# Kernel tuning notes

Measured on AMD Instinct MI355X. Metric: run time of the kernel, lower is better.

## Reference

```python
import jax, jax.numpy as jnp
import numpy as np

N, T, F, H, NH, OUT = 4096, 32, 7, 64, 8, 8


def setup_inputs() -> dict:
    key = jax.random.key(0)
    ks = jax.random.split(key, 24)
    def nrm(k, shape, scale):
        return jax.random.normal(k, shape, jnp.float32) * scale
    s_gru = 1.0 / np.sqrt(H)
    s_gat = 1.0 / np.sqrt(NH * OUT)
    s_lin = 0.05
    return {
        "inputs": jax.random.normal(ks[0], (N, T, F), jnp.float32),
        "adj": jax.random.randint(ks[1], (N, N), 0, 2, jnp.int32),
        "W_ih": nrm(ks[2], (3 * H, F), s_gru),
        "W_hh": nrm(ks[3], (3 * H, H), s_gru),
        "b_ih": nrm(ks[4], (3 * H,), s_gru),
        "b_hh": nrm(ks[5], (3 * H,), s_gru),
        "gat_w": nrm(ks[6], (H, NH * OUT), s_gat),
        "gat_wu": nrm(ks[7], (NH, OUT, 1), 1.0),
        "gat_wv": nrm(ks[8], (NH, OUT, 1), 1.0),
        "gat_bias": nrm(ks[9], (1, NH * OUT), s_gat),
        "proj_w": nrm(ks[10], (NH * OUT, H), s_lin),
        "proj_b": nrm(ks[11], (NH * OUT,), s_lin),
        "mlp_self_w": nrm(ks[12], (H, H), s_lin),
        "mlp_self_b": nrm(ks[13], (H,), s_lin),
        "mlp_pos_w": nrm(ks[14], (H, NH * OUT), s_lin),
        "mlp_pos_b": nrm(ks[15], (H,), s_lin),
        "sem_w1": nrm(ks[16], (H, H), s_lin),
        "sem_b1": nrm(ks[17], (H,), s_lin),
        "sem_w2": nrm(ks[18], (1, H), s_lin),
        "pred_w": nrm(ks[19], (1, H), s_lin),
        "pred_b": nrm(ks[20], (1,), s_lin),
    }


def reference(inputs, adj, W_ih, W_hh, b_ih, b_hh, gat_w, gat_wu, gat_wv,
              gat_bias, proj_w, proj_b, mlp_self_w, mlp_self_b,
              mlp_pos_w, mlp_pos_b, sem_w1, sem_b1, sem_w2, pred_w, pred_b):
    n = inputs.shape[0]
    # --- GRU encoder (batch_first, 1 layer); take final hidden state ---
    gx = jnp.einsum('ntf,gf->tng', inputs, W_ih) + b_ih  # [T, N, 3H]
    h0 = jnp.zeros((n, W_hh.shape[1]), inputs.dtype)

    def step(h, g):
        gh = h @ W_hh.T + b_hh
        gxr, gxz, gxn = jnp.split(g, 3, axis=-1)
        ghr, ghz, ghn = jnp.split(gh, 3, axis=-1)
        r = jax.nn.sigmoid(gxr + ghr)
        z = jax.nn.sigmoid(gxz + ghz)
        nn_ = jnp.tanh(gxn + r * ghn)
        return (1.0 - z) * nn_ + z * h, None

    h, _ = jax.lax.scan(step, h0, gx)  # [N, H]

    # --- multi-head GAT over dense adjacency ---
    sup = (h @ gat_w).reshape(n, NH, OUT).transpose(1, 0, 2)  # [nh, N, out]
    f1 = jnp.einsum('hnd,hdo->hn', sup, gat_wu)[:, None, :]   # [nh, 1, N]
    f2 = jnp.einsum('hnd,hdo->hn', sup, gat_wv)[:, :, None]   # [nh, N, 1]
    logits = jax.nn.leaky_relu(f1 + f2, negative_slope=0.2)   # [nh, N, N]
    adjf = adj.astype(logits.dtype)[None]                     # [1, N, N]
    mw = logits * adjf
    ex = jnp.exp(mw - jnp.max(mw, axis=2, keepdims=True)) * (adjf > 0)
    attn = ex / jnp.clip(jnp.sum(ex, axis=2, keepdims=True), 1e-10)
    pos = jnp.einsum('hij,hjd->hid', attn, sup)               # [nh, N, out]
    pos = pos.transpose(1, 0, 2).reshape(n, NH * OUT)
    pos = pos + gat_bias + h @ proj_w.T + proj_b              # bias + residual proj

    # --- stack self/pos channels, PairNorm (mode='PN') ---
    s = jnp.stack([h @ mlp_self_w.T + mlp_self_b,
                   pos @ mlp_pos_w.T + mlp_pos_b], axis=1)    # [N, 2, H]
    s = s - s.mean(axis=0)
    rownorm_mean = jnp.sqrt(1e-6 + jnp.mean(jnp.sum(s * s, axis=1)))
    s = s / rownorm_mean

    # --- semantic attention over the 2 channels ---
    w = jnp.tanh(s @ sem_w1.T + sem_b1) @ sem_w2.T            # [N, 2, 1]
    we = jnp.exp(w - jnp.max(w, axis=1, keepdims=True))
    beta = we / (jnp.sum(we, axis=1, keepdims=True) + 1e-10)
    emb = jnp.sum(beta * s, axis=1)                           # [N, H]

    # --- predictor ---
    return jax.nn.sigmoid(emb @ pred_w.T + pred_b)            # [N, 1]
```

## Files before the change

### kernel.cpp

```cpp
#include <hip/hip_runtime.h>
#include <math.h>

#define NN 4096
#define TT 32
#define FF 7
#define HH 64
#define NHEAD 8
#define DOUT 8
#define LOG2E 1.44269504f

#if __has_builtin(__builtin_amdgcn_exp2f)
#define EXP2(x) __builtin_amdgcn_exp2f(x)
#else
#define EXP2(x) exp2f(x)
#endif

typedef short bf16x8 __attribute__((ext_vector_type(8)));
typedef float f32x4 __attribute__((ext_vector_type(4)));

__device__ __forceinline__ float sigm(float x){
  x = fminf(fmaxf(x, -30.f), 30.f);
  return 1.f / (1.f + __expf(-x));
}
__device__ __forceinline__ float tanh_fast(float x){
  x = fminf(fmaxf(x, -15.f), 15.f);
  float e = __expf(2.f*x);
  return (e - 1.f) / (e + 1.f);
}
__device__ __forceinline__ unsigned short bf16rne(float f){
  unsigned u = __float_as_uint(f);
  u += 0x7fffu + ((u >> 16) & 1u);
  return (unsigned short)(u >> 16);
}
__device__ __forceinline__ unsigned bfpack2(float a, float b){
  return (unsigned)bf16rne(a) | ((unsigned)bf16rne(b) << 16);
}
__device__ __forceinline__ unsigned cvtpk_bf16(float a, float b){
  unsigned r;
  asm("v_cvt_pk_bf16_f32 %0, %1, %2" : "=v"(r) : "v"(a), "v"(b));
  return r;
}

__global__ __launch_bounds__(256) void k0_prep(
    const float* __restrict__ pw, const float* __restrict__ msw,
    const float* __restrict__ mpw, const float* __restrict__ sw1,
    const float* __restrict__ Wih, const float* __restrict__ Whh,
    const float* __restrict__ bih, const float* __restrict__ bhh,
    float* __restrict__ wtproj, float* __restrict__ wtself,
    float* __restrict__ wtpos, float* __restrict__ wtsem,
    uint4* __restrict__ whhF, uint4* __restrict__ wihF)
{
  if (blockIdx.x < 16){
    int tid = threadIdx.x + blockIdx.x*256;
    int d = tid >> 6, k = tid & 63;
    wtproj[k*64+d] = pw[tid];
    wtself[k*64+d] = msw[tid];
    wtpos[k*64+d]  = mpw[tid];
    wtsem[k*64+d]  = sw1[tid];
    return;
  }
  int idx = (blockIdx.x-16)*256 + threadIdx.x;
  if (idx < 24*64){
    int f = idx >> 6, lane = idx & 63;
    int T = f >> 1, c = f & 1;
    int g = T*16 + (lane & 15);
    const float* wp = Whh + g*64 + c*32 + (lane >> 4)*8;
    uint4 v;
    v.x = bfpack2(wp[0], wp[1]);
    v.y = bfpack2(wp[2], wp[3]);
    v.z = bfpack2(wp[4], wp[5]);
    v.w = bfpack2(wp[6], wp[7]);
    whhF[idx] = v;
  } else if (idx < 36*64){
    int i2 = idx - 24*64;
    int T = i2 >> 6, lane = i2 & 63;
    int g = T*16 + (lane & 15);
    int kg = lane >> 4;
    float bias = (T < 8) ? (bih[g] + bhh[g]) : bih[g];
    float f8[8];
    #pragma unroll
    for (int j = 0; j < 8; ++j){
      int k = kg*8 + j;
      f8[j] = (k < 7) ? Wih[g*7 + k] : ((k == 7) ? bias : 0.f);
    }
    uint4 v;
    v.x = bfpack2(f8[0], f8[1]); v.y = bfpack2(f8[2], f8[3]);
    v.z = bfpack2(f8[4], f8[5]); v.w = bfpack2(f8[6], f8[7]);
    wihF[i2] = v;
  }
}

__global__ __launch_bounds__(256) void k1_fused(
    const float* __restrict__ x,
    const uint4* __restrict__ whhF,
    const uint4* __restrict__ wihF,
    const float* __restrict__ bhh,
    float* __restrict__ hout,
    const int* __restrict__ adj,
    unsigned long long* __restrict__ adjmT)
{
  __shared__ __align__(16) short s_xb[32][16][8];
  __shared__ __align__(16) short s_hb[2][16][72];

  int tid = threadIdx.x;
  int lane = tid & 63, w = tid >> 6;

  if (blockIdx.x >= 256){
    int row = (blockIdx.x - 256)*4 + w;
    const int* ap = adj + (size_t)row*NN;
    size_t base = (size_t)(row >> 4)*1024 + (row & 15);
    #pragma unroll 8
    for (int s = 0; s < 64; ++s){
      unsigned long long m = __ballot(ap[s*64 + lane] != 0);
      if (lane == 0) adjmT[base + s*16] = m;
    }
    return;
  }

  int nb = blockIdx.x * 16;
  int row = lane & 15;
  int kg  = lane >> 4;

  union U { bf16x8 v; uint4 q; };
  U u;
  u.q = wihF[w*64 + lane];           bf16x8 fRx  = u.v;
  u.q = whhF[(w*2+0)*64 + lane];     bf16x8 fRh0 = u.v;
  u.q = whhF[(w*2+1)*64 + lane];     bf16x8 fRh1 = u.v;
  u.q = wihF[(4+w)*64 + lane];       bf16x8 fZx  = u.v;
  u.q = whhF[((4+w)*2+0)*64 + lane]; bf16x8 fZh0 = u.v;
  u.q = whhF[((4+w)*2+1)*64 + lane]; bf16x8 fZh1 = u.v;
  u.q = wihF[(8+w)*64 + lane];       bf16x8 fNx  = u.v;
  u.q = whhF[((8+w)*2+0)*64 + lane]; bf16x8 fNh0 = u.v;
  u.q = whhF[((8+w)*2+1)*64 + lane]; bf16x8 fNh1 = u.v;

  for (int s = tid; s < 4096; s += 256){
    int t = s >> 7, node = (s >> 3) & 15, k = s & 7;
    float v = (k < 7) ? x[(size_t)(nb + node)*224 + t*7 + k] : ((k == 7) ? 1.f : 0.f);
    s_xb[t][node][k] = (short)bf16rne(v);
  }
  for (int i = tid; i < 576; i += 256) ((unsigned*)&s_hb[0][0][0])[i] = 0u;

  float bhn_[4];
  #pragma unroll
  for (int j = 0; j < 4; ++j) bhn_[j] = bhh[128 + w*16 + kg*4 + j];
  float hreg[4] = {0.f, 0.f, 0.f, 0.f};
  f32x4 z4 = {0.f, 0.f, 0.f, 0.f};

  __syncthreads();
  int cur = 0;
  for (int t = 0; t < TT; ++t){
    bf16x8 bx = {0,0,0,0,0,0,0,0};
    if (lane < 16) bx = *(const bf16x8*)&s_xb[t][row][0];
    bf16x8 bh0 = *(const bf16x8*)&s_hb[cur][row][kg*8];
    bf16x8 bh1 = *(const bf16x8*)&s_hb[cur][row][32 + kg*8];

    f32x4 aR = __builtin_amdgcn_mfma_f32_16x16x32_bf16(fRx, bx, z4, 0, 0, 0);
    aR = __builtin_amdgcn_mfma_f32_16x16x32_bf16(fRh0, bh0, aR, 0, 0, 0);
    aR = __builtin_amdgcn_mfma_f32_16x16x32_bf16(fRh1, bh1, aR, 0, 0, 0);
    f32x4 aZ = __builtin_amdgcn_mfma_f32_16x16x32_bf16(fZx, bx, z4, 0, 0, 0);
    aZ = __builtin_amdgcn_mfma_f32_16x16x32_bf16(fZh0, bh0, aZ, 0, 0, 0);
    aZ = __builtin_amdgcn_mfma_f32_16x16x32_bf16(fZh1, bh1, aZ, 0, 0, 0);
    f32x4 aNx = __builtin_amdgcn_mfma_f32_16x16x32_bf16(fNx, bx, z4, 0, 0, 0);
    f32x4 aNh = __builtin_amdgcn_mfma_f32_16x16x32_bf16(fNh0, bh0, z4, 0, 0, 0);
    aNh = __builtin_amdgcn_mfma_f32_16x16x32_bf16(fNh1, bh1, aNh, 0, 0, 0);

    #pragma unroll
    for (int j = 0; j < 4; ++j){
      float rr = sigm(aR[j]);
      float zz = sigm(aZ[j]);
      float nn = tanh_fast(aNx[j] + rr*(aNh[j] + bhn_[j]));
      hreg[j] = (1.f - zz)*nn + zz*hreg[j];
    }
    uint2 p;
    p.x = bfpack2(hreg[0], hreg[1]);
    p.y = bfpack2(hreg[2], hreg[3]);
    *(uint2*)&s_hb[cur^1][row][w*16 + kg*4] = p;
    __syncthreads();
    cur ^= 1;
  }

  #pragma unroll
  for (int j = 0; j < 4; ++j)
    hout[(size_t)(nb + row)*64 + w*16 + kg*4 + j] = hreg[j];
}

__global__ __launch_bounds__(256) void k2_sup(
    const float* __restrict__ h, const float* __restrict__ gat_w,
    const float* __restrict__ wu, const float* __restrict__ wv,
    unsigned short* __restrict__ supbJ,
    float* __restrict__ f1t,
    float* __restrict__ f2)
{
  int tid = threadIdx.x;
  int wave = tid >> 6, lane = tid & 63;
  int n = blockIdx.x*4 + wave;
  float hreg = h[n*64 + lane];
  float acc = 0.f;
  #pragma unroll
  for (int k = 0; k < 64; ++k){
    float hk = __shfl(hreg, k, 64);
    acc += hk * gat_w[k*64 + lane];
  }
  int hh = lane >> 3, o = lane & 7;
  supbJ[(size_t)hh*32768 + (n>>3)*64 + o*8 + (n&7)] = bf16rne(acc);
  float p1 = acc * wu[lane];
  float p2 = acc * wv[lane];
  #pragma unroll
  for (int s = 1; s < 8; s <<= 1){
    p1 += __shfl_xor(p1, s, 64);
    p2 += __shfl_xor(p2, s, 64);
  }
  if (o == 0){
    f1t[(size_t)hh*NN + n] = p1 * LOG2E;
    f2[n*8 + hh] = p2 * LOG2E;
  }
}

__global__ __launch_bounds__(256) void k3_gat(
    const unsigned long long* __restrict__ adjmT,
    const unsigned short* __restrict__ supbJ,
    const float* __restrict__ f1t,
    const float* __restrict__ f2,
    float* __restrict__ posg)
{
  __shared__ f32x4 s_acc[4][64];
  int tid = threadIdx.x;
  int lane = tid & 63, js = tid >> 6;
  int gid = blockIdx.x;
  int ib = gid >> 3, h = gid & 7;
  int i0 = ib*16;
  int col = lane & 15;
  int kg  = lane >> 4;

  float f2v = f2[(size_t)(i0+col)*8 + h];

  const unsigned long long* mrowT = adjmT + (size_t)ib*1024;
  const float* f1p = f1t + (size_t)h*NN;
  const unsigned short* bsrcJ = supbJ + (size_t)h*32768;
  unsigned bge8 = (col >= 8) ? 0xffffffffu : 0u;

  f32x4 acc = {0.f, 0.f, 0.f, 0.f};

  #pragma unroll 4
  for (int cc = 0; cc < 32; ++cc){
    int c = js*32 + cc;
    int j8 = c*32 + kg*8;
    unsigned long long mw = mrowT[(c >> 1)*16 + col];
    unsigned mb = (unsigned)(mw >> (((c & 1) << 5) + (kg << 3)));
    float4 fa = *(const float4*)(f1p + j8);
    float4 fb = *(const float4*)(f1p + j8 + 4);

    float p[8];
    p[0]=fa.x; p[1]=fa.y; p[2]=fa.z; p[3]=fa.w;
    p[4]=fb.x; p[5]=fb.y; p[6]=fb.z; p[7]=fb.w;
    #pragma unroll
    for (int e = 0; e < 8; ++e){
      float ls = p[e] + f2v;
      float lrs = fmaxf(ls, 0.2f*ls);
      float pe = EXP2(lrs);
      p[e] = (mb & (1u << e)) ? pe : 0.f;
    }
    union { bf16x8 v; unsigned u[4]; } A;
    A.u[0] = cvtpk_bf16(p[0], p[1]);
    A.u[1] = cvtpk_bf16(p[2], p[3]);
    A.u[2] = cvtpk_bf16(p[4], p[5]);
    A.u[3] = cvtpk_bf16(p[6], p[7]);

    union { bf16x8 v; uint4 q; } B;
    uint4 ld = *(const uint4*)(bsrcJ + (size_t)(c*4 + kg)*64 + (col & 7)*8);
    B.q.x = bge8 ? 0x3f803f80u : ld.x;
    B.q.y = bge8 ? 0x3f803f80u : ld.y;
    B.q.z = bge8 ? 0x3f803f80u : ld.z;
    B.q.w = bge8 ? 0x3f803f80u : ld.w;

    acc = __builtin_amdgcn_mfma_f32_16x16x32_bf16(A.v, B.v, acc, 0, 0, 0);
  }

  s_acc[js][lane] = acc;
  __syncthreads();
  if (js == 0){
    f32x4 a1 = s_acc[1][lane], a2 = s_acc[2][lane], a3 = s_acc[3][lane];
    #pragma unroll
    for (int j = 0; j < 4; ++j) acc[j] += a1[j] + a2[j] + a3[j];

    int slane = (lane & 48) + 8;
    #pragma unroll
    for (int r4 = 0; r4 < 4; ++r4){
      float sv = __shfl(acc[r4], slane, 64);
      float inv = 1.f / fmaxf(sv, 1e-10f);
      if (col < 8)
        posg[(size_t)(i0 + kg*4 + r4)*64 + h*8 + col] = acc[r4] * inv;
    }
  }
}

__global__ __launch_bounds__(256) void k4_mix(
    const float* __restrict__ h, const float* __restrict__ posg,
    const float* __restrict__ gat_bias, const float* __restrict__ proj_b,
    const float* __restrict__ wtproj, const float* __restrict__ wtself,
    const float* __restrict__ wtpos,
    const float* __restrict__ mlp_self_b, const float* __restrict__ mlp_pos_b,
    float* __restrict__ s0, float* __restrict__ s1, float* __restrict__ part)
{
  int tid = threadIdx.x;
  int wave = tid >> 6, lane = tid & 63;
  int n = blockIdx.x*4 + wave;
  float hreg = h[n*64 + lane];
  float pr = proj_b[lane];
  float se = mlp_self_b[lane];
  #pragma unroll
  for (int k = 0; k < 64; ++k){
    float hk = __shfl(hreg, k, 64);
    pr += hk * wtproj[k*64 + lane];
    se += hk * wtself[k*64 + lane];
  }
  float posf = posg[n*64 + lane] + gat_bias[lane] + pr;
  float s1v = mlp_pos_b[lane];
  #pragma unroll
  for (int k = 0; k < 64; ++k){
    float pk = __shfl(posf, k, 64);
    s1v += pk * wtpos[k*64 + lane];
  }
  s0[n*64+lane] = se;
  s1[n*64+lane] = s1v;

  __shared__ float sb0[4][64];
  __shared__ float sb1[4][64];
  __shared__ float sq[4];
  sb0[wave][lane] = se;
  sb1[wave][lane] = s1v;
  float q = se*se + s1v*s1v;
  #pragma unroll
  for (int s = 1; s < 64; s <<= 1) q += __shfl_xor(q, s, 64);
  if (lane == 0) sq[wave] = q;
  __syncthreads();
  if (tid < 64){
    part[blockIdx.x*130 + tid] = sb0[0][tid]+sb0[1][tid]+sb0[2][tid]+sb0[3][tid];
  } else if (tid < 128){
    int d = tid - 64;
    part[blockIdx.x*130 + 64 + d] = sb1[0][d]+sb1[1][d]+sb1[2][d]+sb1[3][d];
  } else if (tid == 128){
    part[blockIdx.x*130 + 128] = sq[0]+sq[1]+sq[2]+sq[3];
  }
}

__global__ __launch_bounds__(1024) void k5_stats(const float* __restrict__ part, float* __restrict__ stats)
{
  int tid = threadIdx.x;
  __shared__ float s_mu[8][128];
  __shared__ float s_sq[8];
  int c = tid & 127, ch = tid >> 7;
  float a = 0.f;
  for (int b = ch*128; b < ch*128+128; ++b) a += part[b*130 + c];
  s_mu[ch][c] = a;
  if (tid < 8){
    float q = 0.f;
    for (int b = tid*128; b < tid*128+128; ++b) q += part[b*130 + 128];
    s_sq[tid] = q;
  }
  __syncthreads();
  if (tid < 128){
    float m = 0.f;
    #pragma unroll
    for (int j = 0; j < 8; ++j) m += s_mu[j][tid];
    s_mu[0][tid] = m;
    stats[tid] = m / 4096.f;
  }
  __syncthreads();
  if (tid == 0){
    float sq = 0.f;
    #pragma unroll
    for (int j = 0; j < 8; ++j) sq += s_sq[j];
    float mu2 = 0.f;
    for (int i = 0; i < 128; ++i){ float m = s_mu[0][i] / 4096.f; mu2 += m*m; }
    float msq = sq/(4096.f*64.f) - mu2/64.f;
    stats[128] = 1.f / sqrtf(1e-6f + msq);
  }
}

__global__ __launch_bounds__(256) void k6_sem(
    const float* __restrict__ s0, const float* __restrict__ s1,
    const float* __restrict__ stats, const float* __restrict__ wtsem,
    const float* __restrict__ sem_b1, const float* __restrict__ sem_w2,
    const float* __restrict__ pred_w, const float* __restrict__ pred_b,
    float* __restrict__ out)
{
  int tid = threadIdx.x;
  int wave = tid >> 6, lane = tid & 63;
  int n = blockIdx.x*4 + wave;
  float rinv = stats[128];
  float a0 = (s0[n*64+lane] - stats[lane]) * rinv;
  float a1 = (s1[n*64+lane] - stats[64+lane]) * rinv;
  float t0 = sem_b1[lane], t1 = t0;
  #pragma unroll
  for (int k = 0; k < 64; ++k){
    float w = wtsem[k*64 + lane];
    t0 += __shfl(a0, k, 64) * w;
    t1 += __shfl(a1, k, 64) * w;
  }
  t0 = tanh_fast(t0); t1 = tanh_fast(t1);
  float w2 = sem_w2[lane];
  float w0 = t0*w2, w1 = t1*w2;
  #pragma unroll
  for (int s = 1; s < 64; s <<= 1){
    w0 += __shfl_xor(w0, s, 64);
    w1 += __shfl_xor(w1, s, 64);
  }
  float mx = fmaxf(w0, w1);
  float e0 = __expf(w0 - mx), e1 = __expf(w1 - mx);
  float denom = e0 + e1 + 1e-10f;
  float b0 = e0/denom, b1 = e1/denom;
  float emb = b0*a0 + b1*a1;
  float pl = emb * pred_w[lane];
  #pragma unroll
  for (int s = 1; s < 64; s <<= 1) pl += __shfl_xor(pl, s, 64);
  if (lane == 0) out[n] = sigm(pl + pred_b[0]);
}

extern "C" void kernel_launch(void* const* d_in, const int* in_sizes, int n_in,
                              void* d_out, int out_size, void* d_ws, size_t ws_size,
                              hipStream_t stream)
{
  (void)in_sizes; (void)n_in; (void)out_size; (void)ws_size;
  const float* x         = (const float*)d_in[0];
  const int*   adj       = (const int*)d_in[1];
  const float* W_ih      = (const float*)d_in[2];
  const float* W_hh      = (const float*)d_in[3];
  const float* b_ih      = (const float*)d_in[4];
  const float* b_hh      = (const float*)d_in[5];
  const float* gat_w     = (const float*)d_in[6];
  const float* gat_wu    = (const float*)d_in[7];
  const float* gat_wv    = (const float*)d_in[8];
  const float* gat_bias  = (const float*)d_in[9];
  const float* proj_w    = (const float*)d_in[10];
  const float* proj_b    = (const float*)d_in[11];
  const float* mlp_self_w= (const float*)d_in[12];
  const float* mlp_self_b= (const float*)d_in[13];
  const float* mlp_pos_w = (const float*)d_in[14];
  const float* mlp_pos_b = (const float*)d_in[15];
  const float* sem_w1    = (const float*)d_in[16];
  const float* sem_b1    = (const float*)d_in[17];
  const float* sem_w2    = (const float*)d_in[18];
  const float* pred_w    = (const float*)d_in[19];
  const float* pred_b    = (const float*)d_in[20];
  float* out = (float*)d_out;
  float* ws  = (float*)d_ws;

  float* h     = ws + 0;
  unsigned short* supbJ = (unsigned short*)(ws + 262144);
  float* f1t   = ws + 393216;
  float* f2    = ws + 425984;
  uint4* whhF  = (uint4*)(ws + 458752);
  uint4* wihF  = (uint4*)(ws + 464896);
  float* posg  = ws + 589824;
  float* s0    = ws + 851968;
  float* s1    = ws + 1114112;
  unsigned long long* adjmT = (unsigned long long*)(ws + 851968);
  float* part  = ws + 1376256;
  float* stats = ws + 1517576;
  float* wtproj= ws + 1517712;
  float* wtself= wtproj + 4096;
  float* wtpos = wtself + 4096;
  float* wtsem = wtpos  + 4096;

  k0_prep<<<25, 256, 0, stream>>>(proj_w, mlp_self_w, mlp_pos_w, sem_w1,
                                  W_ih, W_hh, b_ih, b_hh,
                                  wtproj, wtself, wtpos, wtsem, whhF, wihF);
  k1_fused<<<1280, 256, 0, stream>>>(x, whhF, wihF, b_hh, h, adj, adjmT);
  k2_sup<<<1024, 256, 0, stream>>>(h, gat_w, gat_wu, gat_wv, supbJ, f1t, f2);
  k3_gat<<<2048, 256, 0, stream>>>(adjmT, supbJ, f1t, f2, posg);
  k4_mix<<<1024, 256, 0, stream>>>(h, posg, gat_bias, proj_b, wtproj, wtself, wtpos,
                                   mlp_self_b, mlp_pos_b, s0, s1, part);
  k5_stats<<<1, 1024, 0, stream>>>(part, stats);
  k6_sem<<<1024, 256, 0, stream>>>(s0, s1, stats, wtsem, sem_b1, sem_w2, pred_w, pred_b, out);
}
```

Measured before the change: 148.1 us.

## Run GRU recurrence in one wave per block and simplify GAT B-operand load

The GRU part of k1_fused now has a single wave hold all the recurrent and input weight fragments in registers and compute all four gate tiles itself. This removes the per-timestep __syncthreads and the double-buffered hidden state, at the cost of each wave doing four times the MFMA and activation work, with three of the four waves exiting early. In k3_gat, the per-element select that swapped in constant ones for the upper 8 columns is replaced by a pointer select into a small ones buffer written by k0_prep, so every lane does a plain vector load. The risks are lower parallelism in the latency-bound GRU loop and heavy register pressure from 36 resident fragments.

```diff
diff --git a/kernel.cpp b/kernel.cpp
--- a/kernel.cpp
+++ b/kernel.cpp
@@ -48,7 +48,8 @@
     const float* __restrict__ bih, const float* __restrict__ bhh,
     float* __restrict__ wtproj, float* __restrict__ wtself,
     float* __restrict__ wtpos, float* __restrict__ wtsem,
-    uint4* __restrict__ whhF, uint4* __restrict__ wihF)
+    uint4* __restrict__ whhF, uint4* __restrict__ wihF,
+    unsigned* __restrict__ onesb)
 {
   if (blockIdx.x < 16){
     int tid = threadIdx.x + blockIdx.x*256;
@@ -59,6 +60,7 @@
     wtsem[k*64+d]  = sw1[tid];
     return;
   }
+  if (blockIdx.x == 16 && threadIdx.x < 32) onesb[threadIdx.x] = 0x3f803f80u;
   int idx = (blockIdx.x-16)*256 + threadIdx.x;
   if (idx < 24*64){
     int f = idx >> 6, lane = idx & 63;
@@ -90,7 +92,7 @@
   }
 }
 
-__global__ __launch_bounds__(256) void k1_fused(
+__global__ __launch_bounds__(256, 1) void k1_fused(
     const float* __restrict__ x,
     const uint4* __restrict__ whhF,
     const uint4* __restrict__ wihF,
@@ -100,7 +102,7 @@
     unsigned long long* __restrict__ adjmT)
 {
   __shared__ __align__(16) short s_xb[32][16][8];
-  __shared__ __align__(16) short s_hb[2][16][72];
+  __shared__ __align__(16) short s_hb[16][72];
 
   int tid = threadIdx.x;
   int lane = tid & 63, w = tid >> 6;
@@ -118,70 +120,85 @@
   }
 
   int nb = blockIdx.x * 16;
-  int row = lane & 15;
-  int kg  = lane >> 4;
-
-  union U { bf16x8 v; uint4 q; };
-  U u;
-  u.q = wihF[w*64 + lane];           bf16x8 fRx  = u.v;
-  u.q = whhF[(w*2+0)*64 + lane];     bf16x8 fRh0 = u.v;
-  u.q = whhF[(w*2+1)*64 + lane];     bf16x8 fRh1 = u.v;
-  u.q = wihF[(4+w)*64 + lane];       bf16x8 fZx  = u.v;
-  u.q = whhF[((4+w)*2+0)*64 + lane]; bf16x8 fZh0 = u.v;
-  u.q = whhF[((4+w)*2+1)*64 + lane]; bf16x8 fZh1 = u.v;
-  u.q = wihF[(8+w)*64 + lane];       bf16x8 fNx  = u.v;
-  u.q = whhF[((8+w)*2+0)*64 + lane]; bf16x8 fNh0 = u.v;
-  u.q = whhF[((8+w)*2+1)*64 + lane]; bf16x8 fNh1 = u.v;
 
   for (int s = tid; s < 4096; s += 256){
     int t = s >> 7, node = (s >> 3) & 15, k = s & 7;
     float v = (k < 7) ? x[(size_t)(nb + node)*224 + t*7 + k] : ((k == 7) ? 1.f : 0.f);
     s_xb[t][node][k] = (short)bf16rne(v);
   }
-  for (int i = tid; i < 576; i += 256) ((unsigned*)&s_hb[0][0][0])[i] = 0u;
-
-  float bhn_[4];
-  #pragma unroll
-  for (int j = 0; j < 4; ++j) bhn_[j] = bhh[128 + w*16 + kg*4 + j];
-  float hreg[4] = {0.f, 0.f, 0.f, 0.f};
+  for (int i = tid; i < 576; i += 256) ((unsigned*)&s_hb[0][0])[i] = 0u;
+  __syncthreads();
+  if (w != 0) return;
+
+  int row = lane & 15;
+  int kg  = lane >> 4;
+
+  union U { bf16x8 v; uint4 q; };
+  bf16x8 whh_f[24];
+  #pragma unroll
+  for (int i = 0; i < 24; ++i){ U u; u.q = whhF[i*64 + lane]; whh_f[i] = u.v; }
+  bf16x8 wih_f[12];
+  #pragma unroll
+  for (int i = 0; i < 12; ++i){ U u; u.q = wihF[i*64 + lane]; wih_f[i] = u.v; }
+  #pragma unroll
+  for (int i = 0; i < 24; ++i) asm volatile("" : "+v"(whh_f[i]));
+  #pragma unroll
+  for (int i = 0; i < 12; ++i) asm volatile("" : "+v"(wih_f[i]));
+
+  float bhn_[4][4];
+  #pragma unroll
+  for (int T = 0; T < 4; ++T)
+    #pragma unroll
+    for (int j = 0; j < 4; ++j)
+      bhn_[T][j] = bhh[128 + T*16 + kg*4 + j];
+
+  float hreg[4][4];
+  #pragma unroll
+  for (int T = 0; T < 4; ++T)
+    #pragma unroll
+    for (int j = 0; j < 4; ++j) hreg[T][j] = 0.f;
+
   f32x4 z4 = {0.f, 0.f, 0.f, 0.f};
 
-  __syncthreads();
-  int cur = 0;
   for (int t = 0; t < TT; ++t){
     bf16x8 bx = {0,0,0,0,0,0,0,0};
     if (lane < 16) bx = *(const bf16x8*)&s_xb[t][row][0];
-    bf16x8 bh0 = *(const bf16x8*)&s_hb[cur][row][kg*8];
-    bf16x8 bh1 = *(const bf16x8*)&s_hb[cur][row][32 + kg*8];
-
-    f32x4 aR = __builtin_amdgcn_mfma_f32_16x16x32_bf16(fRx, bx, z4, 0, 0, 0);
-    aR = __builtin_amdgcn_mfma_f32_16x16x32_bf16(fRh0, bh0, aR, 0, 0, 0);
-    aR = __builtin_amdgcn_mfma_f32_16x16x32_bf16(fRh1, bh1, aR, 0, 0, 0);
-    f32x4 aZ = __builtin_amdgcn_mfma_f32_16x16x32_bf16(fZx, bx, z4, 0, 0, 0);
-    aZ = __builtin_amdgcn_mfma_f32_16x16x32_bf16(fZh0, bh0, aZ, 0, 0, 0);
-    aZ = __builtin_amdgcn_mfma_f32_16x16x32_bf16(fZh1, bh1, aZ, 0, 0, 0);
-    f32x4 aNx = __builtin_amdgcn_mfma_f32_16x16x32_bf16(fNx, bx, z4, 0, 0, 0);
-    f32x4 aNh = __builtin_amdgcn_mfma_f32_16x16x32_bf16(fNh0, bh0, z4, 0, 0, 0);
-    aNh = __builtin_amdgcn_mfma_f32_16x16x32_bf16(fNh1, bh1, aNh, 0, 0, 0);
-
-    #pragma unroll
-    for (int j = 0; j < 4; ++j){
-      float rr = sigm(aR[j]);
-      float zz = sigm(aZ[j]);
-      float nn = tanh_fast(aNx[j] + rr*(aNh[j] + bhn_[j]));
-      hreg[j] = (1.f - zz)*nn + zz*hreg[j];
-    }
-    uint2 p;
-    p.x = bfpack2(hreg[0], hreg[1]);
-    p.y = bfpack2(hreg[2], hreg[3]);
-    *(uint2*)&s_hb[cur^1][row][w*16 + kg*4] = p;
-    __syncthreads();
-    cur ^= 1;
-  }
-
-  #pragma unroll
-  for (int j = 0; j < 4; ++j)
-    hout[(size_t)(nb + row)*64 + w*16 + kg*4 + j] = hreg[j];
+    bf16x8 bh0 = *(const bf16x8*)&s_hb[row][kg*8];
+    bf16x8 bh1 = *(const bf16x8*)&s_hb[row][32 + kg*8];
+
+    #pragma unroll
+    for (int Tr = 0; Tr < 4; ++Tr){
+      f32x4 aR = __builtin_amdgcn_mfma_f32_16x16x32_bf16(wih_f[Tr], bx, z4, 0, 0, 0);
+      aR = __builtin_amdgcn_mfma_f32_16x16x32_bf16(whh_f[Tr*2+0], bh0, aR, 0, 0, 0);
+      aR = __builtin_amdgcn_mfma_f32_16x16x32_bf16(whh_f[Tr*2+1], bh1, aR, 0, 0, 0);
+      f32x4 aZ = __builtin_amdgcn_mfma_f32_16x16x32_bf16(wih_f[4+Tr], bx, z4, 0, 0, 0);
+      aZ = __builtin_amdgcn_mfma_f32_16x16x32_bf16(whh_f[(4+Tr)*2+0], bh0, aZ, 0, 0, 0);
+      aZ = __builtin_amdgcn_mfma_f32_16x16x32_bf16(whh_f[(4+Tr)*2+1], bh1, aZ, 0, 0, 0);
+      f32x4 aNx = __builtin_amdgcn_mfma_f32_16x16x32_bf16(wih_f[8+Tr], bx, z4, 0, 0, 0);
+      f32x4 aNh = __builtin_amdgcn_mfma_f32_16x16x32_bf16(whh_f[(8+Tr)*2+0], bh0, z4, 0, 0, 0);
+      aNh = __builtin_amdgcn_mfma_f32_16x16x32_bf16(whh_f[(8+Tr)*2+1], bh1, aNh, 0, 0, 0);
+      #pragma unroll
+      for (int j = 0; j < 4; ++j){
+        float rr = sigm(aR[j]);
+        float zz = sigm(aZ[j]);
+        float nn = tanh_fast(aNx[j] + rr*(aNh[j] + bhn_[Tr][j]));
+        hreg[Tr][j] = (1.f - zz)*nn + zz*hreg[Tr][j];
+      }
+    }
+    #pragma unroll
+    for (int Tr = 0; Tr < 4; ++Tr){
+      uint2 p;
+      p.x = bfpack2(hreg[Tr][0], hreg[Tr][1]);
+      p.y = bfpack2(hreg[Tr][2], hreg[Tr][3]);
+      *(uint2*)&s_hb[row][Tr*16 + kg*4] = p;
+    }
+  }
+
+  #pragma unroll
+  for (int Tr = 0; Tr < 4; ++Tr)
+    #pragma unroll
+    for (int j = 0; j < 4; ++j)
+      hout[(size_t)(nb + row)*64 + Tr*16 + kg*4 + j] = hreg[Tr][j];
 }
 
 __global__ __launch_bounds__(256) void k2_sup(
@@ -221,6 +238,7 @@
     const unsigned short* __restrict__ supbJ,
     const float* __restrict__ f1t,
     const float* __restrict__ f2,
+    const unsigned short* __restrict__ onesb,
     float* __restrict__ posg)
 {
   __shared__ f32x4 s_acc[4][64];
@@ -236,8 +254,9 @@
 
   const unsigned long long* mrowT = adjmT + (size_t)ib*1024;
   const float* f1p = f1t + (size_t)h*NN;
-  const unsigned short* bsrcJ = supbJ + (size_t)h*32768;
-  unsigned bge8 = (col >= 8) ? 0xffffffffu : 0u;
+  int bmask = (col >= 8) ? 0 : -1;
+  const unsigned short* bbase = (col >= 8) ? onesb
+                                           : (supbJ + (size_t)h*32768 + (col & 7)*8);
 
   f32x4 acc = {0.f, 0.f, 0.f, 0.f};
 
@@ -266,12 +285,9 @@
     A.u[2] = cvtpk_bf16(p[4], p[5]);
     A.u[3] = cvtpk_bf16(p[6], p[7]);
 
+    int boff = ((c*4 + kg) << 6) & bmask;
     union { bf16x8 v; uint4 q; } B;
-    uint4 ld = *(const uint4*)(bsrcJ + (size_t)(c*4 + kg)*64 + (col & 7)*8);
-    B.q.x = bge8 ? 0x3f803f80u : ld.x;
-    B.q.y = bge8 ? 0x3f803f80u : ld.y;
-    B.q.z = bge8 ? 0x3f803f80u : ld.z;
-    B.q.w = bge8 ? 0x3f803f80u : ld.w;
+    B.q = *(const uint4*)(bbase + boff);
 
     acc = __builtin_amdgcn_mfma_f32_16x16x32_bf16(A.v, B.v, acc, 0, 0, 0);
   }
@@ -452,6 +468,7 @@
   float* f2    = ws + 425984;
   uint4* whhF  = (uint4*)(ws + 458752);
   uint4* wihF  = (uint4*)(ws + 464896);
+  unsigned* onesb = (unsigned*)(ws + 475136);
   float* posg  = ws + 589824;
   float* s0    = ws + 851968;
   float* s1    = ws + 1114112;
@@ -465,10 +482,10 @@
 
   k0_prep<<<25, 256, 0, stream>>>(proj_w, mlp_self_w, mlp_pos_w, sem_w1,
                                   W_ih, W_hh, b_ih, b_hh,
-                                  wtproj, wtself, wtpos, wtsem, whhF, wihF);
+                                  wtproj, wtself, wtpos, wtsem, whhF, wihF, onesb);
   k1_fused<<<1280, 256, 0, stream>>>(x, whhF, wihF, b_hh, h, adj, adjmT);
   k2_sup<<<1024, 256, 0, stream>>>(h, gat_w, gat_wu, gat_wv, supbJ, f1t, f2);
-  k3_gat<<<2048, 256, 0, stream>>>(adjmT, supbJ, f1t, f2, posg);
+  k3_gat<<<2048, 256, 0, stream>>>(adjmT, supbJ, f1t, f2, (const unsigned short*)onesb, posg);
   k4_mix<<<1024, 256, 0, stream>>>(h, posg, gat_bias, proj_b, wtproj, wtself, wtpos,
                                    mlp_self_b, mlp_pos_b, s0, s1, part);
   k5_stats<<<1, 1024, 0, stream>>>(part, stats);
```

After: 189.9 us. 1.28x slower.
